# Kernel optimization log

Measured on AMD Instinct MI355X. Metric: run time of the kernel, lower is better.

Reference implementation:

```python
import jax, jax.numpy as jnp
import numpy as np

DIM = 768
HEADS = 12
DIM_HEAD = 64
INNER = HEADS * DIM_HEAD  # 768
EPS = 1e-5


def setup_inputs() -> dict:
    key = jax.random.key(0)
    ks = jax.random.split(key, 5)
    x = jax.random.normal(ks[0], (4, 2048, DIM), dtype=jnp.float32)
    ln_g = jnp.ones((DIM,), dtype=jnp.float32)
    ln_b = jnp.zeros((DIM,), dtype=jnp.float32)
    s1 = 1.0 / np.sqrt(DIM)
    W_qkv = jax.random.uniform(ks[1], (DIM, 3 * INNER), dtype=jnp.float32, minval=-s1, maxval=s1)
    b_qkv = jax.random.uniform(ks[2], (3 * INNER,), dtype=jnp.float32, minval=-s1, maxval=s1)
    s2 = 1.0 / np.sqrt(INNER)
    W_out = jax.random.uniform(ks[3], (INNER, DIM), dtype=jnp.float32, minval=-s2, maxval=s2)
    b_out = jax.random.uniform(ks[4], (DIM,), dtype=jnp.float32, minval=-s2, maxval=s2)
    return {"x": x, "ln_g": ln_g, "ln_b": ln_b, "W_qkv": W_qkv, "b_qkv": b_qkv, "W_out": W_out, "b_out": b_out}


def reference(x, ln_g, ln_b, W_qkv, b_qkv, W_out, b_out):
    b, n, _ = x.shape
    # pre-norm LayerNorm
    mu = jnp.mean(x, axis=-1, keepdims=True)
    var = jnp.mean(jnp.square(x - mu), axis=-1, keepdims=True)
    xn = (x - mu) * jax.lax.rsqrt(var + EPS) * ln_g + ln_b
    qkv = xn @ W_qkv + b_qkv  # [b, n, 3*inner]
    q, k, v = jnp.split(qkv, 3, axis=-1)
    def to_heads(t):
        return t.reshape(b, n, HEADS, DIM_HEAD).transpose(0, 2, 1, 3)  # b h n d
    q, k, v = map(to_heads, (q, k, v))
    q = q * (DIM_HEAD ** -0.5)
    sim = jnp.einsum('bhid,bhjd->bhij', q, k)
    attn = jax.nn.softmax(sim, axis=-1)  # dropout is identity (p=0.0)
    out = jnp.einsum('bhij,bhjd->bhid', attn, v)
    out = out.transpose(0, 2, 1, 3).reshape(b, n, INNER)
    return out @ W_out + b_out
```

## Files before the change

### kernel.cpp

```cpp
#include <hip/hip_runtime.h>
#include <cstdint>
#include <cstddef>


#define SEQ    2048
#define NBATCH 4
#define DMODEL 768
#define NHEADS 12
#define DHEAD  64
#define MROWS  (NBATCH * SEQ)
#define NQKV   (3 * DMODEL)
#define KT     64
#define NT     (SEQ / KT)

using f32x4  = __attribute__((ext_vector_type(4))) float;
using u16x8  = __attribute__((ext_vector_type(8))) unsigned short;
using s16x8  = __attribute__((ext_vector_type(8))) short;

__device__ __forceinline__ unsigned short f2bf(float f) {
  union { float f; unsigned int u; } x; x.f = f;
  unsigned int r = x.u + 0x7fffu + ((x.u >> 16) & 1u);
  return (unsigned short)(r >> 16);
}

#if defined(__has_builtin)
#if __has_builtin(__builtin_amdgcn_cvt_pk_bf16_f32)
#define HAVE_PK_BF16 1
#endif
#if __has_builtin(__builtin_amdgcn_exp2f)
#define HAVE_EXP2 1
#endif
#endif

__device__ __forceinline__ unsigned int pk_bf16(float a, float b) {
#ifdef HAVE_PK_BF16
  auto v = __builtin_amdgcn_cvt_pk_bf16_f32(a, b);
  union { decltype(v) v2; unsigned int u; } c; c.v2 = v; return c.u;
#else
  return (unsigned int)f2bf(a) | ((unsigned int)f2bf(b) << 16);
#endif
}

__device__ __forceinline__ float fexp2(float x) {
#ifdef HAVE_EXP2
  return __builtin_amdgcn_exp2f(x);
#else
  return exp2f(x);
#endif
}

__device__ __forceinline__ f32x4 mfma16(u16x8 a, u16x8 b, f32x4 c) {
  return __builtin_amdgcn_mfma_f32_16x16x32_bf16((s16x8)a, (s16x8)b, c, 0, 0, 0);
}

__device__ __forceinline__ void gl_lds16(const void* g, void* l) {
  __builtin_amdgcn_global_load_lds(
      (const __attribute__((address_space(1))) void*)g,
      (__attribute__((address_space(3))) void*)l, 16, 0, 0);
}

__global__ __launch_bounds__(256) void ln_kernel(
    const float* __restrict__ x, const float* __restrict__ g,
    const float* __restrict__ bb, unsigned short* __restrict__ xn) {
  __shared__ float red[8];
  const int row = blockIdx.x, t = threadIdx.x;
  const float* xr = x + (size_t)row * DMODEL;
  float v0 = xr[t], v1 = xr[t + 256], v2 = xr[t + 512];
  float s = v0 + v1 + v2;
#pragma unroll
  for (int o = 32; o; o >>= 1) s += __shfl_down(s, o);
  if ((t & 63) == 0) red[t >> 6] = s;
  __syncthreads();
  float mu = (red[0] + red[1] + red[2] + red[3]) * (1.0f / DMODEL);
  float d0 = v0 - mu, d1 = v1 - mu, d2 = v2 - mu;
  float q = d0 * d0 + d1 * d1 + d2 * d2;
#pragma unroll
  for (int o = 32; o; o >>= 1) q += __shfl_down(q, o);
  if ((t & 63) == 0) red[4 + (t >> 6)] = q;
  __syncthreads();
  float var = (red[4] + red[5] + red[6] + red[7]) * (1.0f / DMODEL);
  float rstd = rsqrtf(var + 1e-5f);
  size_t base = (size_t)row * DMODEL;
  xn[base + t]       = f2bf(d0 * rstd * g[t]       + bb[t]);
  xn[base + t + 256] = f2bf(d1 * rstd * g[t + 256] + bb[t + 256]);
  xn[base + t + 512] = f2bf(d2 * rstd * g[t + 512] + bb[t + 512]);
}

__global__ __launch_bounds__(256) void tconv_all_kernel(
    const float* __restrict__ Wqkv, unsigned short* __restrict__ Wqkvt,
    const float* __restrict__ Wout, unsigned short* __restrict__ Woutt) {
  __shared__ float tile[32][33];
  const int bx = blockIdx.x;
  const bool isq = bx < 72;
  const float* W = isq ? Wqkv : Wout;
  unsigned short* Wt = isq ? Wqkvt : Woutt;
  const int N = isq ? NQKV : DMODEL;
  const int n0 = (isq ? bx : bx - 72) * 32, k0 = blockIdx.y * 32;
  const int tx = threadIdx.x & 31, ty = threadIdx.x >> 5;
#pragma unroll
  for (int r = 0; r < 4; ++r)
    tile[ty + r * 8][tx] = W[(size_t)(k0 + ty + r * 8) * N + n0 + tx];
  __syncthreads();
#pragma unroll
  for (int r = 0; r < 4; ++r)
    Wt[(size_t)(n0 + ty + r * 8) * DMODEL + k0 + tx] = f2bf(tile[tx][ty + r * 8]);
}

__global__ __launch_bounds__(256, 2) void gemm_qkv_kernel(
    const unsigned short* __restrict__ Wt, const unsigned short* __restrict__ xn,
    const float* __restrict__ bias, unsigned short* __restrict__ qb,
    unsigned short* __restrict__ kb, unsigned short* __restrict__ vt) {
  __shared__ alignas(16) unsigned short As[128 * 64];
  __shared__ alignas(16) unsigned short Bs[128 * 64];
  const int t = threadIdx.x, wid = t >> 6, l = t & 63, quad = l >> 4, ll = l & 15;
  const int bx = blockIdx.x, by = blockIdx.y;
  const bool isv = (bx >= 12);
  const unsigned short* pA;
  const unsigned short* pB;
  int aBase, bBase;
  if (!isv) { pA = Wt; aBase = bx * 128;  pB = xn; bBase = by * 128; }
  else      { pA = xn; aBase = by * 128;  pB = Wt; bBase = 2 * DMODEL + (bx - 12) * 128; }
  const int wa = (wid >> 1) * 64, wb = (wid & 1) * 64;
  const int srow = l >> 3, sblk = (l & 7) ^ srow;
  f32x4 acc[4][4] = {};
  for (int k0 = 0; k0 < DMODEL; k0 += 64) {
#pragma unroll
    for (int cc = 0; cc < 4; ++cc) {
      int call = wid * 4 + cc;
      int r = call * 8 + srow;
      gl_lds16(pA + (size_t)(aBase + r) * DMODEL + k0 + sblk * 8, &As[call * 512]);
      gl_lds16(pB + (size_t)(bBase + r) * DMODEL + k0 + sblk * 8, &Bs[call * 512]);
    }
    __syncthreads();
#pragma unroll
    for (int ks = 0; ks < 2; ++ks) {
      u16x8 af[4], bf[4];
#pragma unroll
      for (int i = 0; i < 4; ++i) {
        int ra = wa + i * 16 + ll, rb = wb + i * 16 + ll;
        int blk = (ks * 4 + quad) ^ (ll & 7);
        af[i] = *(const u16x8*)&As[ra * 64 + blk * 8];
        bf[i] = *(const u16x8*)&Bs[rb * 64 + blk * 8];
      }
#pragma unroll
      for (int mi = 0; mi < 4; ++mi)
#pragma unroll
        for (int ni = 0; ni < 4; ++ni)
          acc[mi][ni] = mfma16(af[mi], bf[ni], acc[mi][ni]);
    }
    __syncthreads();
  }
  if (!isv) {
    const bool isq = (aBase < DMODEL);
    unsigned short* dst = isq ? qb : kb;
    const float sc = isq ? 0.18033688f : 1.0f;
#pragma unroll
    for (int mi = 0; mi < 4; ++mi) {
      int row0 = aBase + wa + mi * 16 + quad * 4;
      float4 bv = *(const float4*)&bias[row0];
      int rr = isq ? row0 : row0 - DMODEL;
      int h = rr >> 6, d0 = rr & 63;
#pragma unroll
      for (int ni = 0; ni < 4; ++ni) {
        int seq = bBase + wb + ni * 16 + ll;
        int b = seq >> 11, i = seq & 2047;
        uint2 pk;
        pk.x = pk_bf16((acc[mi][ni][0] + bv.x) * sc, (acc[mi][ni][1] + bv.y) * sc);
        pk.y = pk_bf16((acc[mi][ni][2] + bv.z) * sc, (acc[mi][ni][3] + bv.w) * sc);
        *(uint2*)&dst[(size_t)((b * NHEADS + h) * SEQ + i) * DHEAD + d0] = pk;
      }
    }
  } else {
#pragma unroll
    for (int mi = 0; mi < 4; ++mi) {
      int gm = aBase + wa + mi * 16 + quad * 4;
      int b = gm >> 11, i0 = gm & 2047;
#pragma unroll
      for (int ni = 0; ni < 4; ++ni) {
        int gn = bBase + wb + ni * 16 + ll;
        float bv = bias[gn];
        int rem = gn - 2 * DMODEL;
        int h = rem >> 6, d = rem & 63;
        int bh = b * NHEADS + h;
        uint2 pk;
        pk.x = pk_bf16(acc[mi][ni][0] + bv, acc[mi][ni][1] + bv);
        pk.y = pk_bf16(acc[mi][ni][2] + bv, acc[mi][ni][3] + bv);
        *(uint2*)&vt[((size_t)bh * DHEAD + d) * SEQ + i0] = pk;
      }
    }
  }
}

__global__ __launch_bounds__(256, 3) void attn_kernel(
    const unsigned short* __restrict__ qbuf, const unsigned short* __restrict__ kbuf,
    const unsigned short* __restrict__ vtg, unsigned short* __restrict__ ao) {
  __shared__ alignas(16) unsigned short stage[2][2][KT * DHEAD];
  __shared__ alignas(16) unsigned short Pws[4][32 * 72];
  const int t = threadIdx.x, wid = t >> 6, l = t & 63, quad = l >> 4, ll = l & 15;
  const int bh = blockIdx.x, qt = blockIdx.y;
  const unsigned short* qg  = qbuf + ((size_t)bh * SEQ + qt * 128) * DHEAD;
  const unsigned short* kg0 = kbuf + (size_t)bh * SEQ * DHEAD;
  const unsigned short* vt0 = vtg  + (size_t)bh * DHEAD * SEQ;
  const int srow = l >> 3;
  const int sblk = (l & 7) ^ srow;

  unsigned short* Qs = &stage[0][0][0];
#pragma unroll
  for (int cc = 0; cc < 4; ++cc) {
    int call = wid * 4 + cc;
    gl_lds16(qg + (call * 8 + srow) * 64 + sblk * 8, Qs + call * 512);
  }
  __syncthreads();
  u16x8 qf[2][2];
#pragma unroll
  for (int mi = 0; mi < 2; ++mi)
#pragma unroll
    for (int ks = 0; ks < 2; ++ks) {
      int r = wid * 32 + mi * 16 + ll;
      int blk = (ks * 4 + quad) ^ (ll & 7);
      qf[mi][ks] = *(const u16x8*)&Qs[r * 64 + blk * 8];
    }
  __syncthreads();

  auto stage_tile = [&](int buf, int kt2) {
    const unsigned short* kg = kg0 + (size_t)kt2 * KT * DHEAD;
#pragma unroll
    for (int c = 0; c < 2; ++c) {
      int call = wid * 2 + c;
      int r = call * 8 + srow;
      gl_lds16(kg + r * 64 + sblk * 8, &stage[buf][0][call * 512]);
      gl_lds16(vt0 + (size_t)r * SEQ + kt2 * KT + sblk * 8, &stage[buf][1][call * 512]);
    }
  };

  f32x4 oacc[2][4] = {};
  float lsum[2] = {0.f, 0.f};
  unsigned short* Pw = Pws[wid];

  stage_tile(0, 0);
  int buf = 0;
  for (int kt2 = 0; kt2 < NT; ++kt2) {
    __syncthreads();
    if (kt2 + 1 < NT) stage_tile(buf ^ 1, kt2 + 1);
    const unsigned short* Ks = &stage[buf][0][0];
    const unsigned short* Vs = &stage[buf][1][0];

    f32x4 st[2][4] = {};
#pragma unroll
    for (int ks = 0; ks < 2; ++ks)
#pragma unroll
      for (int ni = 0; ni < 4; ++ni) {
        int r = ni * 16 + ll;
        int blk = (ks * 4 + quad) ^ (ll & 7);
        u16x8 kf = *(const u16x8*)&Ks[r * 64 + blk * 8];
        st[0][ni] = mfma16(kf, qf[0][ks], st[0][ni]);
        st[1][ni] = mfma16(kf, qf[1][ks], st[1][ni]);
      }

#pragma unroll
    for (int mi = 0; mi < 2; ++mi)
#pragma unroll
      for (int ni = 0; ni < 4; ++ni) {
        float p0 = fexp2(st[mi][ni][0]);
        float p1 = fexp2(st[mi][ni][1]);
        float p2 = fexp2(st[mi][ni][2]);
        float p3 = fexp2(st[mi][ni][3]);
        lsum[mi] += (p0 + p1) + (p2 + p3);
        uint2 pk;
        pk.x = pk_bf16(p0, p1);
        pk.y = pk_bf16(p2, p3);
        *(uint2*)&Pw[(mi * 16 + ll) * 72 + ni * 16 + quad * 4] = pk;
      }
    asm volatile("s_waitcnt lgkmcnt(0)" ::: "memory");

#pragma unroll
    for (int ks = 0; ks < 2; ++ks) {
      u16x8 pf0 = *(const u16x8*)&Pw[(ll) * 72 + ks * 32 + quad * 8];
      u16x8 pf1 = *(const u16x8*)&Pw[(16 + ll) * 72 + ks * 32 + quad * 8];
#pragma unroll
      for (int di = 0; di < 4; ++di) {
        int r = di * 16 + ll;
        int blk = (ks * 4 + quad) ^ (ll & 7);
        u16x8 vf = *(const u16x8*)&Vs[r * 64 + blk * 8];
        oacc[0][di] = mfma16(pf0, vf, oacc[0][di]);
        oacc[1][di] = mfma16(pf1, vf, oacc[1][di]);
      }
    }
    buf ^= 1;
  }

  float lsF[2];
#pragma unroll
  for (int mi = 0; mi < 2; ++mi) {
    float ls = lsum[mi];
    ls += __shfl_xor(ls, 16);
    ls += __shfl_xor(ls, 32);
    lsF[mi] = ls;
  }

  const int b = bh / NHEADS, h = bh - b * NHEADS;
#pragma unroll
  for (int mi = 0; mi < 2; ++mi) {
#pragma unroll
    for (int r = 0; r < 4; ++r) {
      float inv = 1.0f / __shfl(lsF[mi], quad * 4 + r);
      int row = qt * 128 + wid * 32 + mi * 16 + quad * 4 + r;
      size_t base = ((size_t)(b * SEQ + row)) * DMODEL + h * DHEAD;
#pragma unroll
      for (int di = 0; di < 4; ++di)
        ao[base + di * 16 + ll] = f2bf(oacc[mi][di][r] * inv);
    }
  }
}

__global__ __launch_bounds__(256, 2) void gemm_out_kernel(
    const unsigned short* __restrict__ Wt, const unsigned short* __restrict__ ao,
    const float* __restrict__ bias, float* __restrict__ out) {
  __shared__ alignas(16) unsigned short As[64 * 64];
  __shared__ alignas(16) unsigned short Bs[128 * 64];
  const int t = threadIdx.x, wid = t >> 6, l = t & 63, quad = l >> 4, ll = l & 15;
  const int a0 = blockIdx.x * 64;
  const int b0 = blockIdx.y * 128;
  const int wa = (wid >> 1) * 32, wb = (wid & 1) * 64;
  const int srow = l >> 3, sblk = (l & 7) ^ srow;
  f32x4 acc[2][4] = {};
  for (int k0 = 0; k0 < DMODEL; k0 += 64) {
#pragma unroll
    for (int cc = 0; cc < 2; ++cc) {
      int call = wid * 2 + cc;
      int r = call * 8 + srow;
      gl_lds16(Wt + (size_t)(a0 + r) * DMODEL + k0 + sblk * 8, &As[call * 512]);
    }
#pragma unroll
    for (int cc = 0; cc < 4; ++cc) {
      int call = wid * 4 + cc;
      int r = call * 8 + srow;
      gl_lds16(ao + (size_t)(b0 + r) * DMODEL + k0 + sblk * 8, &Bs[call * 512]);
    }
    __syncthreads();
#pragma unroll
    for (int ks = 0; ks < 2; ++ks) {
      u16x8 af[2], bf[4];
#pragma unroll
      for (int i = 0; i < 2; ++i) {
        int ra = wa + i * 16 + ll;
        int blk = (ks * 4 + quad) ^ (ll & 7);
        af[i] = *(const u16x8*)&As[ra * 64 + blk * 8];
      }
#pragma unroll
      for (int i = 0; i < 4; ++i) {
        int rb = wb + i * 16 + ll;
        int blk = (ks * 4 + quad) ^ (ll & 7);
        bf[i] = *(const u16x8*)&Bs[rb * 64 + blk * 8];
      }
#pragma unroll
      for (int mi = 0; mi < 2; ++mi)
#pragma unroll
        for (int ni = 0; ni < 4; ++ni)
          acc[mi][ni] = mfma16(af[mi], bf[ni], acc[mi][ni]);
    }
    __syncthreads();
  }
#pragma unroll
  for (int mi = 0; mi < 2; ++mi) {
    int row0 = a0 + wa + mi * 16 + quad * 4;
    float4 bv = *(const float4*)&bias[row0];
#pragma unroll
    for (int ni = 0; ni < 4; ++ni) {
      int seq = b0 + wb + ni * 16 + ll;
      float4 o;
      o.x = acc[mi][ni][0] + bv.x;
      o.y = acc[mi][ni][1] + bv.y;
      o.z = acc[mi][ni][2] + bv.z;
      o.w = acc[mi][ni][3] + bv.w;
      *(float4*)&out[(size_t)seq * DMODEL + row0] = o;
    }
  }
}

extern "C" void kernel_launch(void* const* d_in, const int* in_sizes, int n_in,
                              void* d_out, int out_size, void* d_ws, size_t ws_size,
                              hipStream_t stream) {
  const float* x     = (const float*)d_in[0];
  const float* ln_g  = (const float*)d_in[1];
  const float* ln_b  = (const float*)d_in[2];
  const float* W_qkv = (const float*)d_in[3];
  const float* b_qkv = (const float*)d_in[4];
  const float* W_out = (const float*)d_in[5];
  const float* b_out = (const float*)d_in[6];
  float* out = (float*)d_out;

  char* ws = (char*)d_ws;
  unsigned short* xn    = (unsigned short*)(ws);
  unsigned short* wqkvt = (unsigned short*)(ws + 12582912);
  unsigned short* woutt = (unsigned short*)(ws + 16121856);
  unsigned short* qb    = (unsigned short*)(ws + 17301504);
  unsigned short* kb    = (unsigned short*)(ws + 29884416);
  unsigned short* vt    = (unsigned short*)(ws + 42467328);
  unsigned short* ao    = xn;

  ln_kernel<<<MROWS, 256, 0, stream>>>(x, ln_g, ln_b, xn);
  tconv_all_kernel<<<dim3(96, 24), 256, 0, stream>>>(W_qkv, wqkvt, W_out, woutt);
  gemm_qkv_kernel<<<dim3(18, 64), 256, 0, stream>>>(wqkvt, xn, b_qkv, qb, kb, vt);
  attn_kernel<<<dim3(NBATCH * NHEADS, SEQ / 128), 256, 0, stream>>>(qb, kb, vt, ao);
  gemm_out_kernel<<<dim3(12, 64), 256, 0, stream>>>(woutt, ao, b_out, out);
}
```

Before: 252.4 us.

## Vectorize LayerNorm per-wave, single-buffer attention tiles, enlarge output GEMM tile

LayerNorm now handles one row per wavefront with float4 loads, wave-level xor reductions and packed bf16 stores, so block-level syncs are gone. The attention kernel drops K/V double buffering to halve shared memory and raise the occupancy hint from 3 to 4 blocks, at the cost of serializing loads with compute behind an extra barrier. The output GEMM doubles its tile along the weight dimension to 128x128 for more reuse per load, halving the grid and raising register use.

```diff
diff --git a/kernel.cpp b/kernel.cpp
--- a/kernel.cpp
+++ b/kernel.cpp
@@ -62,28 +62,40 @@
 __global__ __launch_bounds__(256) void ln_kernel(
     const float* __restrict__ x, const float* __restrict__ g,
     const float* __restrict__ bb, unsigned short* __restrict__ xn) {
-  __shared__ float red[8];
-  const int row = blockIdx.x, t = threadIdx.x;
-  const float* xr = x + (size_t)row * DMODEL;
-  float v0 = xr[t], v1 = xr[t + 256], v2 = xr[t + 512];
-  float s = v0 + v1 + v2;
-#pragma unroll
-  for (int o = 32; o; o >>= 1) s += __shfl_down(s, o);
-  if ((t & 63) == 0) red[t >> 6] = s;
-  __syncthreads();
-  float mu = (red[0] + red[1] + red[2] + red[3]) * (1.0f / DMODEL);
-  float d0 = v0 - mu, d1 = v1 - mu, d2 = v2 - mu;
-  float q = d0 * d0 + d1 * d1 + d2 * d2;
-#pragma unroll
-  for (int o = 32; o; o >>= 1) q += __shfl_down(q, o);
-  if ((t & 63) == 0) red[4 + (t >> 6)] = q;
-  __syncthreads();
-  float var = (red[4] + red[5] + red[6] + red[7]) * (1.0f / DMODEL);
-  float rstd = rsqrtf(var + 1e-5f);
-  size_t base = (size_t)row * DMODEL;
-  xn[base + t]       = f2bf(d0 * rstd * g[t]       + bb[t]);
-  xn[base + t + 256] = f2bf(d1 * rstd * g[t + 256] + bb[t + 256]);
-  xn[base + t + 512] = f2bf(d2 * rstd * g[t + 512] + bb[t + 512]);
+  const int t = threadIdx.x, wid = t >> 6, l = t & 63;
+  const int row = blockIdx.x * 4 + wid;
+  const float4* xr = (const float4*)(x + (size_t)row * DMODEL);
+  const float4* gr = (const float4*)g;
+  const float4* br = (const float4*)bb;
+  float4 v[3];
+#pragma unroll
+  for (int j = 0; j < 3; ++j) v[j] = xr[l + 64 * j];
+  float s = 0.f;
+#pragma unroll
+  for (int j = 0; j < 3; ++j) s += (v[j].x + v[j].y) + (v[j].z + v[j].w);
+#pragma unroll
+  for (int o = 1; o < 64; o <<= 1) s += __shfl_xor(s, o);
+  const float mu = s * (1.0f / DMODEL);
+  float q = 0.f;
+#pragma unroll
+  for (int j = 0; j < 3; ++j) {
+    float a0 = v[j].x - mu, a1 = v[j].y - mu, a2 = v[j].z - mu, a3 = v[j].w - mu;
+    q += (a0 * a0 + a1 * a1) + (a2 * a2 + a3 * a3);
+  }
+#pragma unroll
+  for (int o = 1; o < 64; o <<= 1) q += __shfl_xor(q, o);
+  const float rstd = rsqrtf(q * (1.0f / DMODEL) + 1e-5f);
+  uint2* xo = (uint2*)(xn + (size_t)row * DMODEL);
+#pragma unroll
+  for (int j = 0; j < 3; ++j) {
+    float4 gg = gr[l + 64 * j], bf = br[l + 64 * j];
+    float o0 = (v[j].x - mu) * rstd * gg.x + bf.x;
+    float o1 = (v[j].y - mu) * rstd * gg.y + bf.y;
+    float o2 = (v[j].z - mu) * rstd * gg.z + bf.z;
+    float o3 = (v[j].w - mu) * rstd * gg.w + bf.w;
+    uint2 pk; pk.x = pk_bf16(o0, o1); pk.y = pk_bf16(o2, o3);
+    xo[l + 64 * j] = pk;
+  }
 }
 
 __global__ __launch_bounds__(256) void tconv_all_kernel(
@@ -191,10 +203,10 @@
   }
 }
 
-__global__ __launch_bounds__(256, 3) void attn_kernel(
+__global__ __launch_bounds__(256, 4) void attn_kernel(
     const unsigned short* __restrict__ qbuf, const unsigned short* __restrict__ kbuf,
     const unsigned short* __restrict__ vtg, unsigned short* __restrict__ ao) {
-  __shared__ alignas(16) unsigned short stage[2][2][KT * DHEAD];
+  __shared__ alignas(16) unsigned short stage[2][KT * DHEAD];
   __shared__ alignas(16) unsigned short Pws[4][32 * 72];
   const int t = threadIdx.x, wid = t >> 6, l = t & 63, quad = l >> 4, ll = l & 15;
   const int bh = blockIdx.x, qt = blockIdx.y;
@@ -204,7 +216,7 @@
   const int srow = l >> 3;
   const int sblk = (l & 7) ^ srow;
 
-  unsigned short* Qs = &stage[0][0][0];
+  unsigned short* Qs = &stage[0][0];
 #pragma unroll
   for (int cc = 0; cc < 4; ++cc) {
     int call = wid * 4 + cc;
@@ -220,30 +232,26 @@
       int blk = (ks * 4 + quad) ^ (ll & 7);
       qf[mi][ks] = *(const u16x8*)&Qs[r * 64 + blk * 8];
     }
-  __syncthreads();
-
-  auto stage_tile = [&](int buf, int kt2) {
-    const unsigned short* kg = kg0 + (size_t)kt2 * KT * DHEAD;
-#pragma unroll
-    for (int c = 0; c < 2; ++c) {
-      int call = wid * 2 + c;
-      int r = call * 8 + srow;
-      gl_lds16(kg + r * 64 + sblk * 8, &stage[buf][0][call * 512]);
-      gl_lds16(vt0 + (size_t)r * SEQ + kt2 * KT + sblk * 8, &stage[buf][1][call * 512]);
-    }
-  };
 
   f32x4 oacc[2][4] = {};
   float lsum[2] = {0.f, 0.f};
   unsigned short* Pw = Pws[wid];
 
-  stage_tile(0, 0);
-  int buf = 0;
   for (int kt2 = 0; kt2 < NT; ++kt2) {
     __syncthreads();
-    if (kt2 + 1 < NT) stage_tile(buf ^ 1, kt2 + 1);
-    const unsigned short* Ks = &stage[buf][0][0];
-    const unsigned short* Vs = &stage[buf][1][0];
+    {
+      const unsigned short* kg = kg0 + (size_t)kt2 * KT * DHEAD;
+#pragma unroll
+      for (int c = 0; c < 2; ++c) {
+        int call = wid * 2 + c;
+        int r = call * 8 + srow;
+        gl_lds16(kg + r * 64 + sblk * 8, &stage[0][call * 512]);
+        gl_lds16(vt0 + (size_t)r * SEQ + kt2 * KT + sblk * 8, &stage[1][call * 512]);
+      }
+    }
+    __syncthreads();
+    const unsigned short* Ks = &stage[0][0];
+    const unsigned short* Vs = &stage[1][0];
 
     f32x4 st[2][4] = {};
 #pragma unroll
@@ -286,7 +294,6 @@
         oacc[1][di] = mfma16(pf1, vf, oacc[1][di]);
       }
     }
-    buf ^= 1;
   }
 
   float lsF[2];
@@ -316,45 +323,35 @@
 __global__ __launch_bounds__(256, 2) void gemm_out_kernel(
     const unsigned short* __restrict__ Wt, const unsigned short* __restrict__ ao,
     const float* __restrict__ bias, float* __restrict__ out) {
-  __shared__ alignas(16) unsigned short As[64 * 64];
+  __shared__ alignas(16) unsigned short As[128 * 64];
   __shared__ alignas(16) unsigned short Bs[128 * 64];
   const int t = threadIdx.x, wid = t >> 6, l = t & 63, quad = l >> 4, ll = l & 15;
-  const int a0 = blockIdx.x * 64;
+  const int a0 = blockIdx.x * 128;
   const int b0 = blockIdx.y * 128;
-  const int wa = (wid >> 1) * 32, wb = (wid & 1) * 64;
+  const int wa = (wid >> 1) * 64, wb = (wid & 1) * 64;
   const int srow = l >> 3, sblk = (l & 7) ^ srow;
-  f32x4 acc[2][4] = {};
+  f32x4 acc[4][4] = {};
   for (int k0 = 0; k0 < DMODEL; k0 += 64) {
-#pragma unroll
-    for (int cc = 0; cc < 2; ++cc) {
-      int call = wid * 2 + cc;
-      int r = call * 8 + srow;
-      gl_lds16(Wt + (size_t)(a0 + r) * DMODEL + k0 + sblk * 8, &As[call * 512]);
-    }
 #pragma unroll
     for (int cc = 0; cc < 4; ++cc) {
       int call = wid * 4 + cc;
       int r = call * 8 + srow;
+      gl_lds16(Wt + (size_t)(a0 + r) * DMODEL + k0 + sblk * 8, &As[call * 512]);
       gl_lds16(ao + (size_t)(b0 + r) * DMODEL + k0 + sblk * 8, &Bs[call * 512]);
     }
     __syncthreads();
 #pragma unroll
     for (int ks = 0; ks < 2; ++ks) {
-      u16x8 af[2], bf[4];
-#pragma unroll
-      for (int i = 0; i < 2; ++i) {
-        int ra = wa + i * 16 + ll;
+      u16x8 af[4], bf[4];
+#pragma unroll
+      for (int i = 0; i < 4; ++i) {
+        int ra = wa + i * 16 + ll, rb = wb + i * 16 + ll;
         int blk = (ks * 4 + quad) ^ (ll & 7);
         af[i] = *(const u16x8*)&As[ra * 64 + blk * 8];
-      }
-#pragma unroll
-      for (int i = 0; i < 4; ++i) {
-        int rb = wb + i * 16 + ll;
-        int blk = (ks * 4 + quad) ^ (ll & 7);
         bf[i] = *(const u16x8*)&Bs[rb * 64 + blk * 8];
       }
 #pragma unroll
-      for (int mi = 0; mi < 2; ++mi)
+      for (int mi = 0; mi < 4; ++mi)
 #pragma unroll
         for (int ni = 0; ni < 4; ++ni)
           acc[mi][ni] = mfma16(af[mi], bf[ni], acc[mi][ni]);
@@ -362,7 +359,7 @@
     __syncthreads();
   }
 #pragma unroll
-  for (int mi = 0; mi < 2; ++mi) {
+  for (int mi = 0; mi < 4; ++mi) {
     int row0 = a0 + wa + mi * 16 + quad * 4;
     float4 bv = *(const float4*)&bias[row0];
 #pragma unroll
@@ -399,9 +396,9 @@
   unsigned short* vt    = (unsigned short*)(ws + 42467328);
   unsigned short* ao    = xn;
 
-  ln_kernel<<<MROWS, 256, 0, stream>>>(x, ln_g, ln_b, xn);
+  ln_kernel<<<MROWS / 4, 256, 0, stream>>>(x, ln_g, ln_b, xn);
   tconv_all_kernel<<<dim3(96, 24), 256, 0, stream>>>(W_qkv, wqkvt, W_out, woutt);
   gemm_qkv_kernel<<<dim3(18, 64), 256, 0, stream>>>(wqkvt, xn, b_qkv, qb, kb, vt);
   attn_kernel<<<dim3(NBATCH * NHEADS, SEQ / 128), 256, 0, stream>>>(qb, kb, vt, ao);
-  gemm_out_kernel<<<dim3(12, 64), 256, 0, stream>>>(woutt, ao, b_out, out);
-}
+  gemm_out_kernel<<<dim3(6, 64), 256, 0, stream>>>(woutt, ao, b_out, out);
+}
```

Result: faster. 241.0 us (-4.5%).
